# Kernel optimization log

Hardware: AMD Instinct MI355X
Metric: run time of the kernel (lower is better)

The kernel has to match this reference:

```python
import jax, jax.numpy as jnp
import numpy as np

N_QUBITS = 16   # downsampled_size**2
N_KERNELS = 2
BSZ = 16        # hardcoded BATCH_SIZE in the repo
INV_SQRT2 = 0.70710678118654752


def ry_mat(theta):
    # RY(t) = [[cos(t/2), -sin(t/2)], [sin(t/2), cos(t/2)]]; theta: scalar or any batch shape
    c = jnp.cos(theta / 2)
    s = jnp.sin(theta / 2)
    m = jnp.stack([jnp.stack([c, -s], -1), jnp.stack([s, c], -1)], -2)
    return m.astype(jnp.complex64)


def rx_mat(theta):
    # RX(t) = [[cos(t/2), -i sin(t/2)], [-i sin(t/2), cos(t/2)]]
    c = jnp.cos(theta / 2).astype(jnp.complex64)
    s = jnp.sin(theta / 2).astype(jnp.complex64)
    return jnp.stack([jnp.stack([c, -1j * s], -1), jnp.stack([-1j * s, c], -1)], -2)


def apply_1q(state, U, w, n):
    # state: (b, 2**n) complex; U: (2,2) or (b,2,2); wire 0 = most significant bit
    b = state.shape[0]
    dl, dr = 1 << w, 1 << (n - 1 - w)
    s = state.reshape(b, dl, 2, dr)
    if U.ndim == 2:
        s = jnp.einsum('ab,xLbR->xLaR', U, s)
    else:
        s = jnp.einsum('xab,xLbR->xLaR', U, s)
    return s.reshape(b, -1)


def apply_cnot(state, c, t, n):
    # flip target axis where control bit == 1
    b = state.shape[0]
    st = state.reshape((b,) + (2,) * n)
    flipped = jnp.flip(st, axis=1 + t)
    mshape = [1] * (n + 1)
    mshape[1 + c] = 2
    ctrl = jnp.arange(2).reshape(mshape)
    st = jnp.where(ctrl == 1, flipped, st)
    return st.reshape(b, -1)


def quantum_model(xd, kernel_params):
    # xd: (b, 16) angles; kernel_params: (n_kernels, 5)
    b = xd.shape[0]
    n = N_QUBITS
    N = 1 << n
    bits = (jnp.arange(N)[:, None] >> jnp.arange(n - 1, -1, -1)[None, :]) & 1
    signs = (1 - 2 * bits).astype(jnp.float32)  # (N, n), PauliZ eigenvalues per wire
    enc = ry_mat(xd)  # (b, 16, 2, 2)
    outs = []
    for k in range(N_KERNELS):
        p = kernel_params[k]
        state = jnp.zeros((b, N), jnp.complex64).at[:, 0].set(1.0)
        # encoder: RY(x_i) on wire i
        for w in range(n):
            state = apply_1q(state, enc[:, w], w, n)
        # QuantumConvolution block (shared 5 trainable angles)
        ry0, ry1, ry2 = ry_mat(p[0]), ry_mat(p[1]), ry_mat(p[2])
        rx0, rx1 = rx_mat(p[3]), rx_mat(p[4])
        for i in range(n - 4):
            state = apply_1q(state, ry0, i, n)
            state = apply_cnot(state, i, i + 3, n)
            state = apply_1q(state, ry1, i + 3, n)
            state = apply_1q(state, ry2, i + 1, n)
            state = apply_cnot(state, i + 1, i + 4, n)
            state = apply_cnot(state, i + 3, i + 1, n)
            state = apply_1q(state, rx0, i + 4, n)
            state = apply_1q(state, rx1, i + 1, n)
        for i in range(n - 4):
            state = apply_cnot(state, i + 1, i, n)
            state = apply_cnot(state, i + 3, i, n)
            state = apply_cnot(state, i + 4, i, n)
        probs = state.real ** 2 + state.imag ** 2  # (b, N)
        expz = probs @ signs                        # (b, n)
        outs.append(expz[:, :-4])                   # drop last 4 wires
    return jnp.concatenate(outs, axis=1)            # (b, n_kernels*(n-4)) = (b, 24)


def setup_inputs() -> dict:
    key = jax.random.key(0)
    ks = jax.random.split(key, 8)
    return {
        'x': jax.random.normal(ks[0], (BSZ, 1, 28, 28), jnp.float32),
        'kernel_params': jax.random.uniform(ks[1], (N_KERNELS, 5), jnp.float32) * (2 * np.pi),
        'fc1_w': jax.random.normal(ks[2], (128, 24), jnp.float32) * 0.1,
        'fc1_b': jnp.zeros((128,), jnp.float32),
        'fc2_w': jax.random.normal(ks[3], (64, 128), jnp.float32) * 0.1,
        'fc2_b': jnp.zeros((64,), jnp.float32),
        'fc3_w': jax.random.normal(ks[4], (4, 64), jnp.float32) * 0.1,
        'fc3_b': jnp.zeros((4,), jnp.float32),
    }


def reference(x, kernel_params, fc1_w, fc1_b, fc2_w, fc2_b, fc3_w, fc3_b):
    b = x.shape[0]
    # AvgPool2d(kernel=7, stride=7): 28x28 -> 4x4, then flatten -> 16 features
    xd = x.reshape(b, 1, 4, 7, 4, 7).mean(axis=(3, 5)).reshape(b, 16)
    feats = quantum_model(xd, kernel_params)       # (b, 24)
    h = jax.nn.relu(feats @ fc1_w.T + fc1_b)
    h = jax.nn.relu(h @ fc2_w.T + fc2_b)
    return h @ fc3_w.T + fc3_b                      # (b, 4)
```

## Files before the change

kernel.cpp:

```cpp
#include <hip/hip_runtime.h>
#include <math.h>

typedef __attribute__((ext_vector_type(2))) float f2;

__device__ __forceinline__ f2 pk_mul_c(f2 cs, f2 a){
  f2 d;
  asm("v_pk_mul_f32 %0, %1, %2 op_sel:[0,0] op_sel_hi:[0,1]"
      : "=v"(d) : "v"(cs), "v"(a));
  return d;
}
__device__ __forceinline__ f2 pk_fma_s(f2 cs, f2 b, f2 t){
  f2 d;
  asm("v_pk_fma_f32 %0, %1, %2, %3 op_sel:[1,0,0] op_sel_hi:[1,1,1]"
      : "=v"(d) : "v"(cs), "v"(b), "v"(t));
  return d;
}
__device__ __forceinline__ f2 pk_fma_ns(f2 cs, f2 b, f2 t){
  f2 d;
  asm("v_pk_fma_f32 %0, %1, %2, %3 op_sel:[1,0,0] op_sel_hi:[1,1,1] neg_lo:[1,0,0] neg_hi:[1,0,0]"
      : "=v"(d) : "v"(cs), "v"(b), "v"(t));
  return d;
}
__device__ __forceinline__ f2 pk_fma_sxn(f2 cs, f2 b, f2 t){
  f2 d;
  asm("v_pk_fma_f32 %0, %1, %2, %3 op_sel:[1,1,0] op_sel_hi:[1,0,1] neg_hi:[0,1,0]"
      : "=v"(d) : "v"(cs), "v"(b), "v"(t));
  return d;
}
__device__ __forceinline__ f2 pk_fma_lo(f2 w, f2 b, f2 t){
  f2 d;
  asm("v_pk_fma_f32 %0, %1, %2, %3 op_sel:[0,0,0] op_sel_hi:[0,1,1]"
      : "=v"(d) : "v"(w), "v"(b), "v"(t));
  return d;
}

template<int B> struct LSH {
  static constexpr int v = (B==7)?0 : (B==8)?1 : (B==2)?2 : (B==1)?3 : (B==0)?4 : 5;
};

template<int PB>
__device__ __forceinline__ float lx(float v){
  if constexpr (PB == 7)
    return __int_as_float(__builtin_amdgcn_update_dpp(
        __float_as_int(v), __float_as_int(v), 0xB1, 0xF, 0xF, false));
  else if constexpr (PB == 8)
    return __int_as_float(__builtin_amdgcn_update_dpp(
        __float_as_int(v), __float_as_int(v), 0x4E, 0xF, 0xF, false));
  else if constexpr (PB == 2)
    return __int_as_float(__builtin_amdgcn_ds_swizzle(__float_as_int(v), 0x101F));
  else if constexpr (PB == 1)
    return __int_as_float(__builtin_amdgcn_ds_swizzle(__float_as_int(v), 0x201F));
  else if constexpr (PB == 0)
    return __int_as_float(__builtin_amdgcn_ds_swizzle(__float_as_int(v), 0x401F));
  else
    return __shfl_xor(v, 32, 64);
}

template<int PB, int CB, bool ISRX>
__device__ __forceinline__ void gate_pass(f2* A, f2 cs, int lane)
{
  if constexpr (PB >= 3 && PB <= 6) {
    constexpr int RM = 1 << (PB - 3);
    bool cl = false;
    if constexpr (CB >= 0 && !(CB >= 3 && CB <= 6))
      cl = (lane >> LSH<CB>::v) & 1;
    #pragma unroll
    for (int r = 0; r < 16; ++r) {
      if (r & RM) continue;
      f2 a0 = A[r], a1 = A[r | RM];
      bool sw;
      if constexpr (CB < 0) sw = false;
      else if constexpr (CB >= 3 && CB <= 6) sw = (r >> (CB - 3)) & 1;
      else sw = cl;
      f2 i0, i1;
      i0.x = sw ? a1.x : a0.x;  i0.y = sw ? a1.y : a0.y;
      i1.x = sw ? a0.x : a1.x;  i1.y = sw ? a0.y : a1.y;
      if constexpr (ISRX) {
        A[r]      = pk_fma_sxn(cs, i1, pk_mul_c(cs, i0));
        A[r | RM] = pk_fma_sxn(cs, i0, pk_mul_c(cs, i1));
      } else {
        A[r]      = pk_fma_ns(cs, i1, pk_mul_c(cs, i0));
        A[r | RM] = pk_fma_s (cs, i0, pk_mul_c(cs, i1));
      }
    }
  } else {
    const int mybit = (lane >> LSH<PB>::v) & 1;
    f2 sv;
    if constexpr (!ISRX) {
      float ssy = mybit ? cs.y : -cs.y;
      sv.x = ssy; sv.y = ssy;
    }
    #pragma unroll
    for (int r = 0; r < 16; ++r) {
      f2 p;
      p.x = lx<PB>(A[r].x);
      p.y = lx<PB>(A[r].y);
      bool sw = false;
      if constexpr (CB >= 3 && CB <= 6) sw = (r >> (CB - 3)) & 1;
      f2 u, v;
      u.x = sw ? p.x : A[r].x;  u.y = sw ? p.y : A[r].y;
      v.x = sw ? A[r].x : p.x;  v.y = sw ? A[r].y : p.y;
      if constexpr (ISRX) A[r] = pk_fma_sxn(cs, v, pk_mul_c(cs, u));
      else                A[r] = pk_fma_lo (sv, v, pk_mul_c(cs, u));
    }
  }
}

template<int LO>
__device__ __forceinline__ void iter_reg(f2* A, int lane,
    f2 cs0, f2 cs1, f2 cs2, f2 csx, f2 cs4)
{
  gate_pass<LO+4, -1,   false>(A, cs0, lane);
  gate_pass<LO+1, LO+4, false>(A, cs1, lane);
  gate_pass<LO+3, -1,   false>(A, cs2, lane);
  gate_pass<LO,   LO+3, true >(A, csx, lane);
  gate_pass<LO+3, LO+1, true >(A, cs4, lane);
}

#define RUN6(A) \
  iter_reg<5>(A, lane, cs0,cs1,cs2,csx,cs4); \
  iter_reg<4>(A, lane, cs0,cs1,cs2,csx,cs4); \
  iter_reg<3>(A, lane, cs0,cs1,cs2,csx,cs4); \
  iter_reg<2>(A, lane, cs0,cs1,cs2,csx,cs4); \
  iter_reg<1>(A, lane, cs0,cs1,cs2,csx,cs4); \
  iter_reg<0>(A, lane, cs0,cs1,cs2,csx,cs4);

__device__ __forceinline__ float wave_sum(float v){
  v += lx<7>(v);
  v += lx<8>(v);
  v += lx<2>(v);
  v += lx<1>(v);
  v += lx<0>(v);
  v += __shfl_xor(v, 32, 64);
  return v;
}

#define FLAG_MAGIC 0x5CA1AB1Eu

__global__ __launch_bounds__(256) void sim_kernel(
    const float* __restrict__ x, const float* __restrict__ kp,
    const float* __restrict__ w1, const float* __restrict__ b1,
    const float* __restrict__ w2, const float* __restrict__ b2,
    const float* __restrict__ w3, const float* __restrict__ b3,
    float* __restrict__ pacc,
    float* __restrict__ out)
{
  __shared__ __align__(16) float lds[2048 + 32 + 12 + 48];
  f2*    P    = (f2*)lds;
  float* angw = lds + 2048;
  float* csk  = lds + 2080;
  float* stg  = lds + 2092;

  const int tid = threadIdx.x, wv = tid >> 6, lane = tid & 63;
  const int pair  = blockIdx.x >> 4;
  const int chunk = ((blockIdx.x & 15) << 2) | wv;
  const int k = pair >> 4;
  const int lw = blockIdx.x & 3;

  f2 A[16];

  if (wv == lw){
    {
      int a = lane >> 2, q = lane & 3;
      int ii = a >> 2, jj = a & 3;
      const float* xb = x + (pair & 15)*784 + ii*7*28 + jj*7;
      const float* r0 = xb + q*28;
      float s = r0[0]+r0[1]+r0[2]+r0[3]+r0[4]+r0[5]+r0[6];
      if (q < 3){
        const float* r1 = xb + (q+4)*28;
        s += r1[0]+r1[1]+r1[2]+r1[3]+r1[4]+r1[5]+r1[6];
      }
      s += __shfl_xor(s, 1, 64);
      s += __shfl_xor(s, 2, 64);
      float ang = s * (1.0f/49.0f) * 0.5f;
      if (q == 0){ angw[a*2] = cosf(ang); angw[a*2+1] = sinf(ang); }
    }
    if (lane < 5){
      float a = kp[k*5 + lane] * 0.5f;
      csk[lane*2]   = cosf(a);
      csk[lane*2+1] = sinf(a);
    }
    __threadfence_block();

    f2 cs0 = ((f2*)csk)[0], cs1 = ((f2*)csk)[1], cs2 = ((f2*)csk)[2],
       csx = ((f2*)csk)[3], cs4 = ((f2*)csk)[4];

    {
      float lp = 1.f;
      lp *= ((lane>>5)&1) ? angw[1]  : angw[0];
      lp *= ((lane>>1)&1) ? angw[3]  : angw[2];
      lp *= ( lane    &1) ? angw[5]  : angw[4];
      lp *= ((lane>>2)&1) ? angw[15] : angw[14];
      lp *= ((lane>>3)&1) ? angw[17] : angw[16];
      lp *= ((lane>>4)&1) ? angw[19] : angw[18];
      float c3 = angw[6],  s3 = angw[7];
      float c4w= angw[8],  s4w= angw[9];
      float c5 = angw[10], s5 = angw[11];
      float c6 = angw[12], s6 = angw[13];
      #pragma unroll
      for (int r = 0; r < 16; ++r){
        float rp = ((r&8)? s3:c3) * ((r&4)? s4w:c4w) * ((r&2)? s5:c5) * ((r&1)? s6:c6);
        A[r].x = lp * rp; A[r].y = 0.f;
      }
    }
    RUN6(A);

    #pragma unroll
    for (int r = 0; r < 16; ++r) P[(r << 6) | lane] = A[r];
  }
  __syncthreads();

  f2 cs0 = ((f2*)csk)[0], cs1 = ((f2*)csk)[1], cs2 = ((f2*)csk)[2],
     csx = ((f2*)csk)[3], cs4 = ((f2*)csk)[4];
  {
    int jc = (((lane>>5)&1) << 2) | (((lane>>1)&1) << 1) | (lane & 1);
    int h0 = (chunk << 4) | (jc << 1);
    int r0_ = (h0 >> 3) & 15;
    int l0_ = ((h0>>7)&1) | (((h0>>8)&1)<<1) | (((h0>>2)&1)<<2)
            | (((h0>>1)&1)<<3) | ((h0&1)<<4) | (((h0>>9)&1)<<5);
    f2 ps0 = P[(r0_ << 6) | l0_];
    f2 ps1 = P[(r0_ << 6) | l0_ | 16];

    float c10 = angw[20], s10 = angw[21];
    float c11 = angw[22], s11 = angw[23];
    float c12 = angw[24], s12 = angw[25];
    float preL = 1.f;
    preL *= ((lane>>2)&1) ? angw[27] : angw[26];
    preL *= ((lane>>3)&1) ? angw[29] : angw[28];
    preL *= ((lane>>4)&1) ? angw[31] : angw[30];
    #pragma unroll
    for (int r = 0; r < 16; ++r){
      float f = preL * (((r&4)? s10:c10) * ((r&2)? s11:c11) * ((r&1)? s12:c12));
      f2 v = (r & 8) ? ps1 : ps0;
      A[r].x = v.x * f; A[r].y = v.y * f;
    }
  }

  RUN6(A);

  float out12[12];
  {
    int idx_hi = (chunk << 10)
      | (((lane>>5)&1) << 9) | (((lane>>1)&1) << 8) | ((lane & 1) << 7)
      | (((lane>>2)&1) << 2) | (((lane>>3)&1) << 1) | ((lane>>4)&1);
    float p0[16];
    #pragma unroll
    for (int r = 0; r < 16; ++r) p0[r] = A[r].x*A[r].x + A[r].y*A[r].y;
    float e0[8], d0[8];
    #pragma unroll
    for (int i = 0; i < 8; ++i){ e0[i] = p0[2*i] + p0[2*i+1]; d0[i] = p0[2*i] - p0[2*i+1]; }
    float ee[4], ed[4], de[4], dd[4];
    #pragma unroll
    for (int j = 0; j < 4; ++j){
      ee[j] = e0[2*j] + e0[2*j+1];  ed[j] = e0[2*j] - e0[2*j+1];
      de[j] = d0[2*j] + d0[2*j+1];  dd[j] = d0[2*j] - d0[2*j+1];
    }
    float rT  = (ee[0]+ee[1]) + (ee[2]+ee[3]);
    float r5  = (ee[0]+ee[1]) - (ee[2]+ee[3]);
    float r6  = (ee[0]-ee[1]) - (ee[2]-ee[3]);
    float r7  = (ed[0]-ed[1]) + (ed[2]-ed[3]);
    float r8  = (dd[0]+dd[1]) - (dd[2]+dd[3]);
    float r9  = (de[0]-de[1]) - (de[2]-de[3]);
    float r11 = (dd[0]+dd[1]) + (dd[2]+dd[3]);
    float rsum[12] = {rT,rT,rT,rT,rT, r5, r6, r7, r8, r9, r7, r11};
    #pragma unroll
    for (int w = 0; w < 12; ++w){
      float s = (__popc(idx_hi & (27 << (11 - w))) & 1) ? -rsum[w] : rsum[w];
      out12[w] = wave_sum(s);
    }
  }

  if (lane == 0){
    #pragma unroll
    for (int w = 0; w < 12; ++w) stg[wv*12 + w] = out12[w];
  }
  __syncthreads();
  if (wv == 0){
    if (lane < 12){
      float t = stg[lane] + stg[12+lane] + stg[24+lane] + stg[36+lane];
      pacc[blockIdx.x*16 + lane] = t;
    }
    __threadfence();
    if (lane == 0)
      __hip_atomic_store((unsigned*)(pacc + blockIdx.x*16 + 12), FLAG_MAGIC,
                         __ATOMIC_RELEASE, __HIP_MEMORY_SCOPE_AGENT);
  }

  if ((blockIdx.x >= 256) && ((blockIdx.x & 15) == 15)){
    const int bb = pair & 15;
    if (tid < 32){
      int kk = tid >> 4, cb = tid & 15;
      const unsigned* fp =
          (const unsigned*)(pacc + (((kk*16 + bb)*16 + cb)*16 + 12));
      while (__hip_atomic_load(fp, __ATOMIC_RELAXED, __HIP_MEMORY_SCOPE_AGENT)
             != FLAG_MAGIC)
        __builtin_amdgcn_s_sleep(2);
      __threadfence();
    }
    __syncthreads();

    float* feats = lds;
    float* h1    = lds + 32;
    float* h2    = lds + 160;

    {
      int f = tid >> 3, part = tid & 7;
      if (f < 24){
        int kk = (f >= 12) ? 1 : 0, w = f - kk*12;
        const float* base = pacc + (kk*16 + bb)*256 + w;
        float s = base[part*16] + base[(part+8)*16];
        s += __shfl_xor(s, 1, 64);
        s += __shfl_xor(s, 2, 64);
        s += __shfl_xor(s, 4, 64);
        if (part == 0) feats[f] = s;
      }
    }
    __syncthreads();
    if (tid < 128){
      const float4* wr = (const float4*)(w1 + tid*24);
      const float4* fr = (const float4*)feats;
      float s = b1[tid];
      #pragma unroll
      for (int q = 0; q < 6; ++q){
        float4 a = fr[q], ww = wr[q];
        s += a.x*ww.x + a.y*ww.y + a.z*ww.z + a.w*ww.w;
      }
      h1[tid] = fmaxf(s, 0.f);
    }
    __syncthreads();
    if (tid < 64){
      const float4* wr = (const float4*)(w2 + tid*128);
      const float4* hr = (const float4*)h1;
      float s = b2[tid];
      #pragma unroll
      for (int q = 0; q < 32; ++q){
        float4 a = hr[q], ww = wr[q];
        s += a.x*ww.x + a.y*ww.y + a.z*ww.z + a.w*ww.w;
      }
      h2[tid] = fmaxf(s, 0.f);
    }
    __syncthreads();
    if (tid < 4){
      const float4* wr = (const float4*)(w3 + tid*64);
      const float4* hr = (const float4*)h2;
      float s = b3[tid];
      #pragma unroll
      for (int q = 0; q < 16; ++q){
        float4 a = hr[q], ww = wr[q];
        s += a.x*ww.x + a.y*ww.y + a.z*ww.z + a.w*ww.w;
      }
      out[bb*4 + tid] = s;
    }
  }
}

extern "C" void kernel_launch(void* const* d_in, const int* in_sizes, int n_in,
                              void* d_out, int out_size, void* d_ws, size_t ws_size,
                              hipStream_t stream) {
  const float* x  = (const float*)d_in[0];
  const float* kp = (const float*)d_in[1];
  const float* w1 = (const float*)d_in[2];
  const float* b1 = (const float*)d_in[3];
  const float* w2 = (const float*)d_in[4];
  const float* b2 = (const float*)d_in[5];
  const float* w3 = (const float*)d_in[6];
  const float* b3 = (const float*)d_in[7];
  float* out  = (float*)d_out;
  float* pacc = (float*)d_ws;

  sim_kernel<<<512, 256, 0, stream>>>(x, kp, w1, b1, w2, b2, w3, b3, pacc, out);
}
```

Baseline: 95.36 us.

## Replace fence-based cross-block handoff with relaxed system-scope atomics and in-wave reduction

Producer blocks now write their 12 partial sums as six 64-bit system-scope relaxed atomic stores, wait on vmcnt, then set the flag with a relaxed store. This replaces the __threadfence and release store. Consumer threads each poll one flag, read that row with atomic loads and reduce all 12 features across 16 lanes with shuffles, removing the fence, a barrier and the separate gather pass. One ds_swizzle lane exchange also becomes a DPP row-rotate. The relaxed ordering drops the release/acquire guarantees, so correctness now depends on vmcnt waits and system-scope coherence, and the DPP 0x128 pattern must give the same partner lane as the old swizzle.

Measured after the change: 85.48 us, median of 2. -10.4%, faster.

```diff
diff --git a/kernel.cpp b/kernel.cpp
--- a/kernel.cpp
+++ b/kernel.cpp
@@ -49,7 +49,8 @@
   else if constexpr (PB == 2)
     return __int_as_float(__builtin_amdgcn_ds_swizzle(__float_as_int(v), 0x101F));
   else if constexpr (PB == 1)
-    return __int_as_float(__builtin_amdgcn_ds_swizzle(__float_as_int(v), 0x201F));
+    return __int_as_float(__builtin_amdgcn_update_dpp(
+        __float_as_int(v), __float_as_int(v), 0x128, 0xF, 0xF, false));
   else if constexpr (PB == 0)
     return __int_as_float(__builtin_amdgcn_ds_swizzle(__float_as_int(v), 0x401F));
   else
@@ -142,8 +143,7 @@
     const float* __restrict__ w1, const float* __restrict__ b1,
     const float* __restrict__ w2, const float* __restrict__ b2,
     const float* __restrict__ w3, const float* __restrict__ b3,
-    float* __restrict__ pacc,
-    float* __restrict__ out)
+    float* __restrict__ pacc, float* __restrict__ out)
 {
   __shared__ __align__(16) float lds[2048 + 32 + 12 + 48];
   f2*    P    = (f2*)lds;
@@ -276,46 +276,55 @@
   }
   __syncthreads();
   if (wv == 0){
-    if (lane < 12){
-      float t = stg[lane] + stg[12+lane] + stg[24+lane] + stg[36+lane];
-      pacc[blockIdx.x*16 + lane] = t;
-    }
-    __threadfence();
+    if (lane < 6){
+      int w0 = 2*lane, w1 = w0 + 1;
+      float t0 = stg[w0] + stg[12+w0] + stg[24+w0] + stg[36+w0];
+      float t1 = stg[w1] + stg[12+w1] + stg[24+w1] + stg[36+w1];
+      unsigned long long v = ((unsigned long long)__float_as_uint(t1) << 32)
+                           |  (unsigned long long)__float_as_uint(t0);
+      __hip_atomic_store((unsigned long long*)(pacc + blockIdx.x*16) + lane, v,
+                         __ATOMIC_RELAXED, __HIP_MEMORY_SCOPE_SYSTEM);
+    }
+    asm volatile("s_waitcnt vmcnt(0)" ::: "memory");
     if (lane == 0)
       __hip_atomic_store((unsigned*)(pacc + blockIdx.x*16 + 12), FLAG_MAGIC,
-                         __ATOMIC_RELEASE, __HIP_MEMORY_SCOPE_AGENT);
+                         __ATOMIC_RELAXED, __HIP_MEMORY_SCOPE_SYSTEM);
   }
 
   if ((blockIdx.x >= 256) && ((blockIdx.x & 15) == 15)){
     const int bb = pair & 15;
-    if (tid < 32){
-      int kk = tid >> 4, cb = tid & 15;
-      const unsigned* fp =
-          (const unsigned*)(pacc + (((kk*16 + bb)*16 + cb)*16 + 12));
-      while (__hip_atomic_load(fp, __ATOMIC_RELAXED, __HIP_MEMORY_SCOPE_AGENT)
-             != FLAG_MAGIC)
-        __builtin_amdgcn_s_sleep(2);
-      __threadfence();
-    }
-    __syncthreads();
-
     float* feats = lds;
     float* h1    = lds + 32;
     float* h2    = lds + 160;
 
-    {
-      int f = tid >> 3, part = tid & 7;
-      if (f < 24){
-        int kk = (f >= 12) ? 1 : 0, w = f - kk*12;
-        const float* base = pacc + (kk*16 + bb)*256 + w;
-        float s = base[part*16] + base[(part+8)*16];
-        s += __shfl_xor(s, 1, 64);
-        s += __shfl_xor(s, 2, 64);
-        s += __shfl_xor(s, 4, 64);
-        if (part == 0) feats[f] = s;
+    if (tid < 32){
+      int kk = tid >> 4, cb = tid & 15;
+      float* prow = pacc + ((kk*16 + bb)*16 + cb)*16;
+      const unsigned* fp = (const unsigned*)(prow + 12);
+      while (__hip_atomic_load(fp, __ATOMIC_RELAXED, __HIP_MEMORY_SCOPE_SYSTEM)
+             != FLAG_MAGIC)
+        __builtin_amdgcn_s_sleep(8);
+      asm volatile("" ::: "memory");
+      float f[12];
+      #pragma unroll
+      for (int q = 0; q < 6; ++q){
+        unsigned long long v = __hip_atomic_load(
+            (const unsigned long long*)prow + q,
+            __ATOMIC_RELAXED, __HIP_MEMORY_SCOPE_SYSTEM);
+        f[2*q]   = __uint_as_float((unsigned)v);
+        f[2*q+1] = __uint_as_float((unsigned)(v >> 32));
+      }
+      #pragma unroll
+      for (int m = 1; m <= 8; m <<= 1)
+        #pragma unroll
+        for (int w = 0; w < 12; ++w) f[w] += __shfl_xor(f[w], m, 64);
+      if (cb == 0){
+        #pragma unroll
+        for (int w = 0; w < 12; ++w) feats[kk*12 + w] = f[w];
       }
     }
     __syncthreads();
+
     if (tid < 128){
       const float4* wr = (const float4*)(w1 + tid*24);
       const float4* fr = (const float4*)feats;
```
